# Optimization experiments

Hardware: AMD Instinct MI355X
Metric: run time of the kernel (lower is better)

## Reference

```python
import jax, jax.numpy as jnp
import numpy as np

TF = 512  # text_features
VF = 512  # video_features


def setup_inputs() -> dict:
    key = jax.random.key(0)
    k1, k2, k3 = jax.random.split(key, 3)
    text = jax.random.normal(k1, (4, 32, TF), dtype=jnp.float32)
    video = jax.random.normal(k2, (4, 64, 196, VF), dtype=jnp.float32)
    # nn.Linear(text_features + video_features, 1): weight (1, TF+VF), bias (1,)
    w = jax.random.normal(k3, (TF + VF,), dtype=jnp.float32) * (1.0 / np.sqrt(TF + VF))
    b = jnp.zeros((1,), dtype=jnp.float32)
    return {"text": text, "video": video, "w": w, "b": b}


def reference(text, video, w, b):
    # Split the 1-output linear over the concat into text-only and video-only
    # projections: Linear(cat([t, v])) = t @ wt + v @ wv + b  (exact algebra).
    tf = text.shape[-1]
    wt, wv = w[:tf], w[tf:]
    score_t = jnp.einsum('btf,f->bt', text, wt) + b[0]        # (B, St)
    score_v = jnp.einsum('bvhf,f->bvh', video, wv)            # (B, Sv, HW)
    scores = score_t[:, :, None, None] + score_v[:, None]     # (B, St, Sv, HW)
    B, St, Sv, HW = scores.shape
    # softmax over the flattened (Sv*HW) dim, per (b, st)
    weights = jax.nn.softmax(scores.reshape(B, St, Sv * HW), axis=-1)
    weights = weights.reshape(B, St, Sv, HW)
    # fused[b,st,sv,f] = sum_hw weights[b,st,sv,hw] * video[b,sv,hw,f]
    fused = jnp.einsum('bsvh,bvhf->bsvf', weights, video)
    return fused
```

## Files before the change

kernel.cpp:

```cpp
#include <hip/hip_runtime.h>

#define TF 512
#define VF 512
#define BB 4
#define ST 32
#define SV 64
#define HW 196
#define ROWS_PER_B (SV * HW)
#define NROW (BB * ROWS_PER_B)
#define PART_PER_B (ROWS_PER_B / 4)

__global__ __launch_bounds__(256) void score_kernel(const float4* __restrict__ video,
                                                    const float* __restrict__ w,
                                                    float* __restrict__ escore,
                                                    float* __restrict__ partial) {
    int tid   = threadIdx.x;
    int gwave = (blockIdx.x * 256 + tid) >> 6;
    int lane  = tid & 63;
    const float4* row = video + (size_t)gwave * (VF / 4);
    const float4* wv4 = (const float4*)(w + TF);
    float4 a0 = row[lane];
    float4 a1 = row[lane + 64];
    float4 w0 = wv4[lane];
    float4 w1 = wv4[lane + 64];
    float s = a0.x * w0.x + a0.y * w0.y + a0.z * w0.z + a0.w * w0.w
            + a1.x * w1.x + a1.y * w1.y + a1.z * w1.z + a1.w * w1.w;
    #pragma unroll
    for (int off = 32; off > 0; off >>= 1)
        s += __shfl_down(s, off, 64);

    __shared__ float ps[4];
    if (lane == 0) {
        float e = __expf(s);
        escore[gwave] = e;
        ps[tid >> 6] = e;
    }
    __syncthreads();
    if (tid == 0)
        partial[blockIdx.x] = ps[0] + ps[1] + ps[2] + ps[3];
}

__global__ __launch_bounds__(512) void fuse_kernel(const float4* __restrict__ video,
                                                   const float* __restrict__ escore,
                                                   const float* __restrict__ partial,
                                                   float4* __restrict__ out) {
    int bv  = blockIdx.x;
    int b   = bv >> 6;
    int v   = bv & 63;
    int tid = threadIdx.x;

    __shared__ float red[8];
    __shared__ float wsh[HW];
    __shared__ float4 accsh[4][128];

    const float* pb = partial + b * PART_PER_B;
    float local = 0.0f;
    for (int i = tid; i < PART_PER_B; i += 512) local += pb[i];
    #pragma unroll
    for (int off = 32; off > 0; off >>= 1) local += __shfl_down(local, off, 64);
    if ((tid & 63) == 0) red[tid >> 6] = local;

    if (tid < HW) wsh[tid] = escore[bv * HW + tid];
    __syncthreads();

    float tot = red[0] + red[1] + red[2] + red[3]
              + red[4] + red[5] + red[6] + red[7];
    float inv = 1.0f / tot;

    const float4* vrow = video + (size_t)bv * HW * (VF / 4);
    int f = tid & 127;
    int q = tid >> 7;
    float4 acc = make_float4(0.f, 0.f, 0.f, 0.f);
    for (int h = q; h < HW; h += 4) {
        float wh = wsh[h];
        float4 x = vrow[h * (VF / 4) + f];
        acc.x = fmaf(wh, x.x, acc.x);
        acc.y = fmaf(wh, x.y, acc.y);
        acc.z = fmaf(wh, x.z, acc.z);
        acc.w = fmaf(wh, x.w, acc.w);
    }
    accsh[q][f] = acc;
    __syncthreads();

    float4 r0 = accsh[0][f], r1 = accsh[1][f], r2 = accsh[2][f], r3 = accsh[3][f];
    float4 res;
    res.x = (r0.x + r1.x + r2.x + r3.x) * inv;
    res.y = (r0.y + r1.y + r2.y + r3.y) * inv;
    res.z = (r0.z + r1.z + r2.z + r3.z) * inv;
    res.w = (r0.w + r1.w + r2.w + r3.w) * inv;

    #pragma unroll
    for (int s = 0; s < 8; s++) {
        size_t idx = (((size_t)(b * ST + q * 8 + s)) * SV + v) * (VF / 4) + f;
        out[idx] = res;
    }
}

extern "C" void kernel_launch(void* const* d_in, const int* in_sizes, int n_in,
                              void* d_out, int out_size, void* d_ws, size_t ws_size,
                              hipStream_t stream) {
    const float* video = (const float*)d_in[1];
    const float* w     = (const float*)d_in[2];
    float* escore  = (float*)d_ws;
    float* partial = escore + NROW;

    score_kernel<<<NROW / 4, 256, 0, stream>>>((const float4*)video, w,
                                               escore, partial);
    fuse_kernel<<<BB * SV, 512, 0, stream>>>((const float4*)video, escore,
                                             partial, (float4*)d_out);
}
```

Before: 174.3 us.

## Fuse score, exp and weighted accumulation into a single pass over video

Computes the per-row score, exponentiates it, and accumulates exp-weighted video rows in the same kernel, so video is read once instead of twice. Partial accumulators over four HW segments per (b,v) are written to workspace, and a small second kernel sums them, normalises by the per-batch denominator and broadcasts to all text positions. This removes the escore round trip and the second full read of video. In exchange, each wave serially walks rows with a shuffle reduction per row, and the per-block parallelism is lower.

```diff
diff --git a/kernel.cpp b/kernel.cpp
--- a/kernel.cpp
+++ b/kernel.cpp
@@ -6,93 +6,105 @@
 #define ST 32
 #define SV 64
 #define HW 196
-#define ROWS_PER_B (SV * HW)
-#define NROW (BB * ROWS_PER_B)
-#define PART_PER_B (ROWS_PER_B / 4)
+#define NBV (BB * SV)
+#define NSEG 4
+#define SEGH (HW / NSEG)
 
-__global__ __launch_bounds__(256) void score_kernel(const float4* __restrict__ video,
-                                                    const float* __restrict__ w,
-                                                    float* __restrict__ escore,
-                                                    float* __restrict__ partial) {
-    int tid   = threadIdx.x;
-    int gwave = (blockIdx.x * 256 + tid) >> 6;
-    int lane  = tid & 63;
-    const float4* row = video + (size_t)gwave * (VF / 4);
+
+__global__ __launch_bounds__(256) void score_acc_kernel(const float4* __restrict__ video,
+                                                        const float* __restrict__ w,
+                                                        float4* __restrict__ Gpart,
+                                                        float* __restrict__ dpart) {
+    int bv   = blockIdx.x >> 2;
+    int seg  = blockIdx.x & 3;
+    int tid  = threadIdx.x;
+    int wave = tid >> 6;
+    int lane = tid & 63;
+
     const float4* wv4 = (const float4*)(w + TF);
-    float4 a0 = row[lane];
-    float4 a1 = row[lane + 64];
     float4 w0 = wv4[lane];
     float4 w1 = wv4[lane + 64];
-    float s = a0.x * w0.x + a0.y * w0.y + a0.z * w0.z + a0.w * w0.w
-            + a1.x * w1.x + a1.y * w1.y + a1.z * w1.z + a1.w * w1.w;
-    #pragma unroll
-    for (int off = 32; off > 0; off >>= 1)
-        s += __shfl_down(s, off, 64);
 
-    __shared__ float ps[4];
-    if (lane == 0) {
+    const float4* vbase = video + ((size_t)bv * HW + seg * SEGH) * (VF / 4);
+
+    float4 acc0 = make_float4(0.f, 0.f, 0.f, 0.f);
+    float4 acc1 = make_float4(0.f, 0.f, 0.f, 0.f);
+    float  esum = 0.f;
+
+    #pragma unroll 2
+    for (int hl = wave; hl < SEGH; hl += 4) {
+        const float4* row = vbase + hl * (VF / 4);
+        float4 x0 = row[lane];
+        float4 x1 = row[lane + 64];
+        float s = x0.x * w0.x + x0.y * w0.y + x0.z * w0.z + x0.w * w0.w
+                + x1.x * w1.x + x1.y * w1.y + x1.z * w1.z + x1.w * w1.w;
+        #pragma unroll
+        for (int off = 32; off > 0; off >>= 1)
+            s += __shfl_xor(s, off, 64);
         float e = __expf(s);
-        escore[gwave] = e;
-        ps[tid >> 6] = e;
+        esum += e;
+        acc0.x = fmaf(e, x0.x, acc0.x);
+        acc0.y = fmaf(e, x0.y, acc0.y);
+        acc0.z = fmaf(e, x0.z, acc0.z);
+        acc0.w = fmaf(e, x0.w, acc0.w);
+        acc1.x = fmaf(e, x1.x, acc1.x);
+        acc1.y = fmaf(e, x1.y, acc1.y);
+        acc1.z = fmaf(e, x1.z, acc1.z);
+        acc1.w = fmaf(e, x1.w, acc1.w);
     }
+
+    __shared__ float4 sacc[4][VF / 4];
+    __shared__ float  sd[4];
+    sacc[wave][lane]      = acc0;
+    sacc[wave][lane + 64] = acc1;
+    if (lane == 0) sd[wave] = esum;
     __syncthreads();
-    if (tid == 0)
-        partial[blockIdx.x] = ps[0] + ps[1] + ps[2] + ps[3];
+
+    int c = tid & 127, half = tid >> 7;
+    float4 a  = sacc[half * 2][c];
+    float4 bq = sacc[half * 2 + 1][c];
+    float4 t  = make_float4(a.x + bq.x, a.y + bq.y, a.z + bq.z, a.w + bq.w);
+    sacc[half * 2][c] = t;
+    __syncthreads();
+    if (half == 0) {
+        float4 u = sacc[2][c];
+        Gpart[((size_t)seg * NBV + bv) * (VF / 4) + c] =
+            make_float4(t.x + u.x, t.y + u.y, t.z + u.z, t.w + u.w);
+    }
+    if (tid == 0) dpart[blockIdx.x] = sd[0] + sd[1] + sd[2] + sd[3];
 }
 
-__global__ __launch_bounds__(512) void fuse_kernel(const float4* __restrict__ video,
-                                                   const float* __restrict__ escore,
-                                                   const float* __restrict__ partial,
-                                                   float4* __restrict__ out) {
+__global__ __launch_bounds__(256) void out_kernel(const float4* __restrict__ Gpart,
+                                                  const float* __restrict__ dpart,
+                                                  float4* __restrict__ out) {
     int bv  = blockIdx.x;
     int b   = bv >> 6;
     int v   = bv & 63;
     int tid = threadIdx.x;
 
-    __shared__ float red[8];
-    __shared__ float wsh[HW];
-    __shared__ float4 accsh[4][128];
+    __shared__ float  red[4];
+    __shared__ float4 gsh[2][VF / 4];
 
-    const float* pb = partial + b * PART_PER_B;
-    float local = 0.0f;
-    for (int i = tid; i < PART_PER_B; i += 512) local += pb[i];
+    float val = dpart[b * 256 + tid];
     #pragma unroll
-    for (int off = 32; off > 0; off >>= 1) local += __shfl_down(local, off, 64);
-    if ((tid & 63) == 0) red[tid >> 6] = local;
+    for (int off = 32; off > 0; off >>= 1) val += __shfl_xor(val, off, 64);
+    if ((tid & 63) == 0) red[tid >> 6] = val;
 
-    if (tid < HW) wsh[tid] = escore[bv * HW + tid];
+    int c = tid & 127, half = tid >> 7;
+    float4 g0 = Gpart[((size_t)(half * 2) * NBV + bv) * (VF / 4) + c];
+    float4 g1 = Gpart[((size_t)(half * 2 + 1) * NBV + bv) * (VF / 4) + c];
+    gsh[half][c] = make_float4(g0.x + g1.x, g0.y + g1.y, g0.z + g1.z, g0.w + g1.w);
     __syncthreads();
 
-    float tot = red[0] + red[1] + red[2] + red[3]
-              + red[4] + red[5] + red[6] + red[7];
-    float inv = 1.0f / tot;
-
-    const float4* vrow = video + (size_t)bv * HW * (VF / 4);
-    int f = tid & 127;
-    int q = tid >> 7;
-    float4 acc = make_float4(0.f, 0.f, 0.f, 0.f);
-    for (int h = q; h < HW; h += 4) {
-        float wh = wsh[h];
-        float4 x = vrow[h * (VF / 4) + f];
-        acc.x = fmaf(wh, x.x, acc.x);
-        acc.y = fmaf(wh, x.y, acc.y);
-        acc.z = fmaf(wh, x.z, acc.z);
-        acc.w = fmaf(wh, x.w, acc.w);
-    }
-    accsh[q][f] = acc;
-    __syncthreads();
-
-    float4 r0 = accsh[0][f], r1 = accsh[1][f], r2 = accsh[2][f], r3 = accsh[3][f];
-    float4 res;
-    res.x = (r0.x + r1.x + r2.x + r3.x) * inv;
-    res.y = (r0.y + r1.y + r2.y + r3.y) * inv;
-    res.z = (r0.z + r1.z + r2.z + r3.z) * inv;
-    res.w = (r0.w + r1.w + r2.w + r3.w) * inv;
+    float inv = 1.0f / (red[0] + red[1] + red[2] + red[3]);
+    float4 o0 = gsh[0][c], o1 = gsh[1][c];
+    float4 res = make_float4((o0.x + o1.x) * inv, (o0.y + o1.y) * inv,
+                             (o0.z + o1.z) * inv, (o0.w + o1.w) * inv);
 
     #pragma unroll
-    for (int s = 0; s < 8; s++) {
-        size_t idx = (((size_t)(b * ST + q * 8 + s)) * SV + v) * (VF / 4) + f;
-        out[idx] = res;
+    for (int k = 0; k < 16; k++) {
+        int s = half * 16 + k;
+        out[(((size_t)(b * ST + s)) * SV + v) * (VF / 4) + c] = res;
     }
 }
 
@@ -101,11 +113,10 @@
                               hipStream_t stream) {
     const float* video = (const float*)d_in[1];
     const float* w     = (const float*)d_in[2];
-    float* escore  = (float*)d_ws;
-    float* partial = escore + NROW;
+    float4* Gpart = (float4*)d_ws;
+    float*  dpart = (float*)((char*)d_ws + (size_t)NSEG * NBV * (VF / 4) * sizeof(float4));
 
-    score_kernel<<<NROW / 4, 256, 0, stream>>>((const float4*)video, w,
-                                               escore, partial);
-    fuse_kernel<<<BB * SV, 512, 0, stream>>>((const float4*)video, escore,
-                                             partial, (float4*)d_out);
+    score_acc_kernel<<<NBV * NSEG, 256, 0, stream>>>((const float4*)video, w,
+                                                     Gpart, dpart);
+    out_kernel<<<NBV, 256, 0, stream>>>(Gpart, dpart, (float4*)d_out);
 }
```

Result: faster. 165.6 us (-5.0%).
